# Performance work log

Hardware: AMD Instinct MI355X
Metric: run time of the kernel (lower is better)

The kernel has to match this reference:

```python
import jax, jax.numpy as jnp
import numpy as np

NC, CIN, COUT = 10000, 64, 64      # coarse points, inChans, outChans
CH = COUT // 2                     # up_conv / skip channels
NCONVS, TMP = 2, 2                 # nConvs, temp_mp_skip
GX = GY = GT = 64                  # coarse grid
FX, FY, FT = 2 * GX, 2 * GY, GT    # fine grid after [2,2,1] upsample
NF = 4 * NC                        # fine points (2x2x1 expansion per coarse voxel)
BN_EPS = 1e-5


def _build_maps():
    """Build MinkowskiEngine-style kernel maps (in_idx, out_idx) for a 3x3x3
    stride-1 sparse conv on the fine coordinate set. Padded with NF (dummy)."""
    rng = np.random.default_rng(0)
    lin = rng.choice(GX * GY * GT, size=NC, replace=False)
    cx, cy, ct = np.unravel_index(lin, (GX, GY, GT))
    coarse = np.stack([cx, cy, ct], 1).astype(np.int64)
    # transpose-conv output coords: each coarse voxel emits a 2x2x1 block,
    # offset order fixed and matched by the einsum in reference()
    offs4 = np.array([[0, 0, 0], [0, 1, 0], [1, 0, 0], [1, 1, 0]])
    fine = (coarse[:, None, :] * np.array([2, 2, 1]) + offs4[None]).reshape(-1, 3)
    table = -np.ones(FX * FY * FT, np.int64)
    keys = fine[:, 0] * (FY * FT) + fine[:, 1] * FT + fine[:, 2]
    table[keys] = np.arange(NF)
    offs = np.array([[dx, dy, dt] for dx in (-1, 0, 1)
                     for dy in (-1, 0, 1) for dt in (-1, 0, 1)])
    pin, pout = [], []
    for o in offs:
        nb = fine + o
        ok = (nb >= 0).all(1) & (nb[:, 0] < FX) & (nb[:, 1] < FY) & (nb[:, 2] < FT)
        k2 = np.clip(nb[:, 0] * (FY * FT) + nb[:, 1] * FT + nb[:, 2], 0, table.size - 1)
        idx = np.where(ok, table[k2], -1)
        m = idx >= 0
        pin.append(idx[m].astype(np.int32))
        pout.append(np.nonzero(m)[0].astype(np.int32))
    mmax = max(len(p) for p in pin)
    in_idx = np.full((27, mmax), NF, np.int32)
    out_idx = np.full((27, mmax), NF, np.int32)
    for k in range(27):
        n = len(pin[k])
        in_idx[k, :n] = pin[k]
        out_idx[k, :n] = pout[k]
    return jnp.asarray(in_idx), jnp.asarray(out_idx)


def sparse_conv(x, w, in_idx, out_idx):
    """gather -> GEMM -> scatter-add. x:[NF,Cin], w:[27,Cin,Cout]."""
    xp = jnp.concatenate([x, jnp.zeros((1, x.shape[1]), x.dtype)], 0)
    g = xp[in_idx]                                   # [27, M, Cin]
    c = jnp.einsum('kmc,kco->kmo', g, w)             # [27, M, Cout]
    out = jnp.zeros((NF + 1, w.shape[-1]), x.dtype)
    out = out.at[out_idx.reshape(-1)].add(c.reshape(-1, w.shape[-1]))
    return out[:NF]


def batch_norm(x, gamma, beta):
    m = x.mean(0)
    v = jnp.var(x, axis=0)
    return (x - m) * jax.lax.rsqrt(v + BN_EPS) * gamma + beta


def setup_inputs() -> dict:
    key = jax.random.key(0)
    ks = jax.random.split(key, 5)
    in_idx, out_idx = _build_maps()
    s = 0.05
    return {
        'x_feats': jax.random.normal(ks[0], (NC, CIN), jnp.float32),
        'skip_feats': jax.random.normal(ks[1], (NF * TMP, CH), jnp.float32),
        'w_up': jax.random.normal(ks[2], (4, CIN, CIN), jnp.float32) * s,
        'w_upconv': jax.random.normal(ks[3], (27, CIN, CH), jnp.float32) * s,
        'bn1_gamma': jnp.ones((CH,), jnp.float32),
        'bn1_beta': jnp.zeros((CH,), jnp.float32),
        'convs_w': jax.random.normal(ks[4], (NCONVS, 27, COUT, COUT), jnp.float32) * s,
        'convs_gamma': jnp.ones((NCONVS, COUT), jnp.float32),
        'convs_beta': jnp.zeros((NCONVS, COUT), jnp.float32),
        'in_idx': in_idx,
        'out_idx': out_idx,
    }


def reference(x_feats, skip_feats, w_up, w_upconv, bn1_gamma, bn1_beta,
              convs_w, convs_gamma, convs_beta, in_idx, out_idx):
    # MinkowskiConvolutionTranspose kernel=stride=[2,2,1]: each coarse point
    # emits 4 fine points (offset order matches _build_maps).
    up = jnp.einsum('nc,kco->nko', x_feats, w_up).reshape(NF, CIN)  # [NF, CIN]
    out = jax.nn.elu(batch_norm(sparse_conv(up, w_upconv, in_idx, out_idx),
                                bn1_gamma, bn1_beta))               # [NF, CH]
    # MinkowskiMaxPooling kernel=stride=[1,1,TMP] over the temporal axis
    skip = skip_feats.reshape(NF, TMP, CH).max(axis=1)              # [NF, CH]
    xcat = jnp.concatenate([out, skip], axis=1)                     # [NF, COUT]
    h = xcat
    for i in range(NCONVS):  # LUConv: ELU(BN(conv(x)))
        h = jax.nn.elu(batch_norm(sparse_conv(h, convs_w[i], in_idx, out_idx),
                                  convs_gamma[i], convs_beta[i]))
    return jax.nn.elu(h + xcat)
```

## Files before the change

### kernel.cpp

```cpp
#include <hip/hip_runtime.h>
#include <math.h>


__device__ __forceinline__ float elu(float v) { return v > 0.f ? v : expm1f(v); }

__device__ __forceinline__ float4 f4add(float4 a, float4 b) {
  return make_float4(a.x + b.x, a.y + b.y, a.z + b.z, a.w + b.w);
}

__global__ void __launch_bounds__(256) k_init(int* __restrict__ pos, float* __restrict__ stats,
                                              float* __restrict__ upz, float* __restrict__ xcz,
                                              int n_pos) {
  int i = blockIdx.x * blockDim.x + threadIdx.x;
  for (int j = i; j < n_pos; j += gridDim.x * blockDim.x) pos[j] = -1;
  if (i < 384) stats[i] = 0.f;
  if (i < 64) { upz[i] = 0.f; xcz[i] = 0.f; }
}

__global__ void k_meta(const int* __restrict__ in_idx, int mmax, int NF,
                       int* __restrict__ cnt, int* __restrict__ base) {
  __shared__ int sc[27];
  int k = threadIdx.x;
  if (k < 27) {
    int lo = 0, hi = mmax;
    while (lo < hi) {
      int mid = (lo + hi) >> 1;
      if (in_idx[(size_t)k * mmax + mid] >= NF) hi = mid; else lo = mid + 1;
    }
    sc[k] = lo;
    cnt[k] = lo;
  }
  __syncthreads();
  if (threadIdx.x == 0) {
    int acc = 0;
    for (int j = 0; j < 27; ++j) { base[j] = acc; acc += (sc[j] + 127) & ~127; }
    base[27] = acc;
  }
}

__global__ void __launch_bounds__(256) k_scatter(const int* __restrict__ out_idx, int mmax, int NF,
                                                 const int* __restrict__ cnt, const int* __restrict__ base,
                                                 int* __restrict__ pos) {
  int k = blockIdx.y;
  int m = blockIdx.x * blockDim.x + threadIdx.x;
  if (m >= cnt[k]) return;
  pos[(size_t)k * NF + out_idx[(size_t)k * mmax + m]] = base[k] + m;
}

template <int RU>
__global__ void __launch_bounds__(256) k_up(const float* __restrict__ x, const float* __restrict__ w_up,
                                            float* __restrict__ up, int NC) {
  const int lane = threadIdx.x & 63;
  const int j = threadIdx.x >> 6;
  float wreg[64];
#pragma unroll
  for (int ci = 0; ci < 64; ++ci) wreg[ci] = w_up[(size_t)(j * 64 + ci) * 64 + lane];
  const int n0 = blockIdx.x * RU;
#pragma unroll
  for (int r = 0; r < RU; ++r) {
    int n = n0 + r;
    if (n >= NC) break;
    const float* xr = x + (size_t)n * 64;
    float a0 = 0.f, a1 = 0.f, a2 = 0.f, a3 = 0.f;
#pragma unroll
    for (int ci = 0; ci < 64; ci += 4) {
      a0 = fmaf(xr[ci + 0], wreg[ci + 0], a0);
      a1 = fmaf(xr[ci + 1], wreg[ci + 1], a1);
      a2 = fmaf(xr[ci + 2], wreg[ci + 2], a2);
      a3 = fmaf(xr[ci + 3], wreg[ci + 3], a3);
    }
    up[(size_t)(n * 4 + j) * 64 + lane] = (a0 + a1) + (a2 + a3);
  }
}

template <int COUT>
__global__ void __launch_bounds__(256) k_gemm2(const float* __restrict__ x,
                                               const float* __restrict__ w,
                                               const int* __restrict__ in_idx, int mmax, int NF,
                                               const int* __restrict__ cnt, const int* __restrict__ base,
                                               float* __restrict__ Cbuf) {
  constexpr int CW = COUT / 16;
  constexpr int STA = 68;
  __shared__ float At[64 * STA];
  __shared__ float Ws[64 * COUT];
  __shared__ int sidx[64];

  const int k = blockIdx.y;
  const int ck = cnt[k];
  const int m0 = blockIdx.x * 64;
  if (m0 >= ck) return;
  const int tid = threadIdx.x;

  if (tid < 64) {
    int m = m0 + tid;
    sidx[tid] = (m < ck) ? in_idx[(size_t)k * mmax + m] : NF;
  }
  {
    const float4* wsrc = (const float4*)(w + (size_t)k * 64 * COUT);
    float4* wdst = (float4*)Ws;
#pragma unroll
    for (int p = 0; p < 64 * COUT / 4 / 256; ++p) wdst[tid + p * 256] = wsrc[tid + p * 256];
  }
  __syncthreads();
  {
    const int r0 = tid & 15;
    const int cb = tid >> 4;
#pragma unroll
    for (int p = 0; p < 4; ++p) {
      int row = r0 + p * 16;
      float4 v = *(const float4*)(x + (size_t)sidx[row] * 64 + cb * 4);
      At[(cb * 4 + 0) * STA + row] = v.x;
      At[(cb * 4 + 1) * STA + row] = v.y;
      At[(cb * 4 + 2) * STA + row] = v.z;
      At[(cb * 4 + 3) * STA + row] = v.w;
    }
  }
  __syncthreads();

  const int mi = tid >> 4;
  const int ci = tid & 15;
  float acc[4][CW];
#pragma unroll
  for (int i = 0; i < 4; ++i)
#pragma unroll
    for (int j = 0; j < CW; ++j) acc[i][j] = 0.f;

#pragma unroll 4
  for (int kk = 0; kk < 64; ++kk) {
    float4 a = *(const float4*)(At + kk * STA + mi * 4);
    const float* brow = Ws + kk * COUT + ci * CW;
    float b[CW];
#pragma unroll
    for (int j = 0; j < CW; ++j) b[j] = brow[j];
    float av[4] = {a.x, a.y, a.z, a.w};
#pragma unroll
    for (int i = 0; i < 4; ++i)
#pragma unroll
      for (int j = 0; j < CW; ++j) acc[i][j] = fmaf(av[i], b[j], acc[i][j]);
  }

  const int bk = base[k];
#pragma unroll
  for (int i = 0; i < 4; ++i) {
    float* dst = Cbuf + (size_t)(bk + m0 + mi * 4 + i) * COUT + ci * CW;
#pragma unroll
    for (int j = 0; j < CW; ++j) dst[j] = acc[i][j];
  }
}

template <int COUT>
__global__ void __launch_bounds__(256) k_red(const float* __restrict__ Cbuf, const int* __restrict__ pos,
                                             float* __restrict__ y, float* __restrict__ s1,
                                             float* __restrict__ s2, int NF) {
  constexpr int C4 = COUT / 4;
  const int c4 = threadIdx.x & (C4 - 1);
  const int rl = threadIdx.x / C4;
  const int rpb = 256 / C4;
  float4 p1 = make_float4(0, 0, 0, 0), p2 = make_float4(0, 0, 0, 0);
  for (int o = blockIdx.x * rpb + rl; o < NF; o += gridDim.x * rpb) {
    float4 acc = make_float4(0, 0, 0, 0);
#pragma unroll
    for (int k = 0; k < 27; ++k) {
      int p = pos[(size_t)k * NF + o];
      if (p >= 0) {
        float4 v = *(const float4*)(Cbuf + (size_t)p * COUT + c4 * 4);
        acc = f4add(acc, v);
      }
    }
    *(float4*)(y + (size_t)o * COUT + c4 * 4) = acc;
    p1 = f4add(p1, acc);
    p2 = f4add(p2, make_float4(acc.x * acc.x, acc.y * acc.y, acc.z * acc.z, acc.w * acc.w));
  }
  __shared__ float4 sh[256];
  sh[threadIdx.x] = p1;
  __syncthreads();
  if (rl == 0) {
    float4 t = make_float4(0, 0, 0, 0);
    for (int r = 0; r < rpb; ++r) t = f4add(t, sh[r * C4 + c4]);
    atomicAdd(s1 + c4 * 4 + 0, t.x); atomicAdd(s1 + c4 * 4 + 1, t.y);
    atomicAdd(s1 + c4 * 4 + 2, t.z); atomicAdd(s1 + c4 * 4 + 3, t.w);
  }
  __syncthreads();
  sh[threadIdx.x] = p2;
  __syncthreads();
  if (rl == 0) {
    float4 t = make_float4(0, 0, 0, 0);
    for (int r = 0; r < rpb; ++r) t = f4add(t, sh[r * C4 + c4]);
    atomicAdd(s2 + c4 * 4 + 0, t.x); atomicAdd(s2 + c4 * 4 + 1, t.y);
    atomicAdd(s2 + c4 * 4 + 2, t.z); atomicAdd(s2 + c4 * 4 + 3, t.w);
  }
}

__global__ void __launch_bounds__(256) k_xcat(const float* __restrict__ y1, const float* __restrict__ skip,
                                              const float* __restrict__ gamma, const float* __restrict__ beta,
                                              const float* __restrict__ s1, const float* __restrict__ s2,
                                              float* __restrict__ xcat, int NF) {
  int t = blockIdx.x * blockDim.x + threadIdx.x;
  if (t >= NF * 32) return;
  int c = t & 31, o = t >> 5;
  float invn = 1.f / (float)NF;
  float m = s1[c] * invn;
  float var = s2[c] * invn - m * m;
  float sc = rsqrtf(var + 1e-5f) * gamma[c];
  float v = (y1[(size_t)o * 32 + c] - m) * sc + beta[c];
  xcat[(size_t)o * 64 + c] = elu(v);
  float a = skip[((size_t)o * 2) * 32 + c];
  float b = skip[((size_t)o * 2 + 1) * 32 + c];
  xcat[(size_t)o * 64 + 32 + c] = fmaxf(a, b);
}

__global__ void __launch_bounds__(256) k_norm(const float* __restrict__ y, const float* __restrict__ gamma,
                                              const float* __restrict__ beta, const float* __restrict__ s1,
                                              const float* __restrict__ s2, float* __restrict__ h, int NF) {
  int t = blockIdx.x * blockDim.x + threadIdx.x;
  if (t >= NF * 64) return;
  int c = t & 63;
  float invn = 1.f / (float)NF;
  float m = s1[c] * invn;
  float var = s2[c] * invn - m * m;
  float sc = rsqrtf(var + 1e-5f) * gamma[c];
  h[t] = elu((y[t] - m) * sc + beta[c]);
}

__global__ void __launch_bounds__(256) k_final(const float* __restrict__ y, const float* __restrict__ gamma,
                                               const float* __restrict__ beta, const float* __restrict__ s1,
                                               const float* __restrict__ s2, const float* __restrict__ xcat,
                                               float* __restrict__ out, int NF) {
  int t = blockIdx.x * blockDim.x + threadIdx.x;
  if (t >= NF * 64) return;
  int c = t & 63;
  float invn = 1.f / (float)NF;
  float m = s1[c] * invn;
  float var = s2[c] * invn - m * m;
  float sc = rsqrtf(var + 1e-5f) * gamma[c];
  float v = elu((y[t] - m) * sc + beta[c]);
  out[t] = elu(v + xcat[t]);
}

extern "C" void kernel_launch(void* const* d_in, const int* in_sizes, int n_in,
                              void* d_out, int out_size, void* d_ws, size_t ws_size,
                              hipStream_t stream) {
  const float* x_feats  = (const float*)d_in[0];
  const float* skip     = (const float*)d_in[1];
  const float* w_up     = (const float*)d_in[2];
  const float* w_upconv = (const float*)d_in[3];
  const float* bn1_g    = (const float*)d_in[4];
  const float* bn1_b    = (const float*)d_in[5];
  const float* convs_w  = (const float*)d_in[6];
  const float* convs_g  = (const float*)d_in[7];
  const float* convs_b  = (const float*)d_in[8];
  const int*   in_idx   = (const int*)d_in[9];
  const int*   out_idx  = (const int*)d_in[10];

  const int NC = in_sizes[0] / 64;
  const int NF = 4 * NC;
  const int mmax = in_sizes[9] / 27;

  char* ws = (char*)d_ws;
  size_t off = 0;
  auto alloc = [&](size_t bytes) -> void* {
    void* p = ws + off;
    off += (bytes + 255) & ~(size_t)255;
    return p;
  };
  int*   pos   = (int*)alloc((size_t)27 * NF * 4);
  int*   cnt   = (int*)alloc(32 * 4);
  int*   basep = (int*)alloc(32 * 4);
  float* stats = (float*)alloc(384 * 4);
  float* up    = (float*)alloc(((size_t)NF + 1) * 64 * 4);
  float* xcat  = (float*)alloc(((size_t)NF + 1) * 64 * 4);
  float* y     = (float*)alloc((size_t)NF * 64 * 4);
  float* Cb    = (float*)(ws + off);
  float* h     = up;

  k_init<<<1024, 256, 0, stream>>>(pos, stats, up + (size_t)NF * 64,
                                   xcat + (size_t)NF * 64, 27 * NF);
  k_meta<<<1, 64, 0, stream>>>(in_idx, mmax, NF, cnt, basep);
  dim3 gs((mmax + 255) / 256, 27);
  k_scatter<<<gs, 256, 0, stream>>>(out_idx, mmax, NF, cnt, basep, pos);
  k_up<16><<<(NC + 15) / 16, 256, 0, stream>>>(x_feats, w_up, up, NC);

  dim3 gg((mmax + 63) / 64, 27);
  k_gemm2<32><<<gg, 256, 0, stream>>>(up, w_upconv, in_idx, mmax, NF, cnt, basep, Cb);
  k_red<32><<<320, 256, 0, stream>>>(Cb, pos, y, stats + 0, stats + 64, NF);
  k_xcat<<<(NF * 32 + 255) / 256, 256, 0, stream>>>(y, skip, bn1_g, bn1_b,
                                                    stats + 0, stats + 64, xcat, NF);
  k_gemm2<64><<<gg, 256, 0, stream>>>(xcat, convs_w, in_idx, mmax, NF, cnt, basep, Cb);
  k_red<64><<<640, 256, 0, stream>>>(Cb, pos, y, stats + 128, stats + 192, NF);
  k_norm<<<(NF * 64 + 255) / 256, 256, 0, stream>>>(y, convs_g, convs_b,
                                                    stats + 128, stats + 192, h, NF);
  k_gemm2<64><<<gg, 256, 0, stream>>>(h, convs_w + 27 * 64 * 64, in_idx, mmax, NF, cnt, basep, Cb);
  k_red<64><<<640, 256, 0, stream>>>(Cb, pos, y, stats + 256, stats + 320, NF);
  k_final<<<(NF * 64 + 255) / 256, 256, 0, stream>>>(y, convs_g + 64, convs_b + 64,
                                                     stats + 256, stats + 320, xcat,
                                                     (float*)d_out, NF);
}
```

Measured before the change: 459.6 us.

## Replace dense per-offset position map with compact per-output neighbor lists

The dense 27xNF position table, which needed filling with -1 and scanning over all 27 offsets for every output row, is replaced by a per-output degree counter plus a list of up to 32 neighbor entries built with atomics. The reduction kernels now loop only over the real neighbors of each output, cutting index reads and branches. Grid sizes for the reduction and init kernels also change so there is one row group per block. Atomic insertion makes the summation order nondeterministic, which can perturb floating-point results slightly, and the list size assumes at most 32 neighbors per output.

New measurement: 791.8 us. 1.72x slower.

```diff
diff --git a/kernel.cpp b/kernel.cpp
--- a/kernel.cpp
+++ b/kernel.cpp
@@ -8,11 +8,11 @@
   return make_float4(a.x + b.x, a.y + b.y, a.z + b.z, a.w + b.w);
 }
 
-__global__ void __launch_bounds__(256) k_init(int* __restrict__ pos, float* __restrict__ stats,
+__global__ void __launch_bounds__(256) k_init(int* __restrict__ deg, float* __restrict__ stats,
                                               float* __restrict__ upz, float* __restrict__ xcz,
-                                              int n_pos) {
+                                              int NF) {
   int i = blockIdx.x * blockDim.x + threadIdx.x;
-  for (int j = i; j < n_pos; j += gridDim.x * blockDim.x) pos[j] = -1;
+  for (int j = i; j < NF; j += gridDim.x * blockDim.x) deg[j] = 0;
   if (i < 384) stats[i] = 0.f;
   if (i < 64) { upz[i] = 0.f; xcz[i] = 0.f; }
 }
@@ -38,13 +38,15 @@
   }
 }
 
-__global__ void __launch_bounds__(256) k_scatter(const int* __restrict__ out_idx, int mmax, int NF,
-                                                 const int* __restrict__ cnt, const int* __restrict__ base,
-                                                 int* __restrict__ pos) {
+__global__ void __launch_bounds__(256) k_scatter2(const int* __restrict__ out_idx, int mmax,
+                                                  const int* __restrict__ cnt, const int* __restrict__ base,
+                                                  int* __restrict__ deg, int* __restrict__ ent) {
   int k = blockIdx.y;
   int m = blockIdx.x * blockDim.x + threadIdx.x;
   if (m >= cnt[k]) return;
-  pos[(size_t)k * NF + out_idx[(size_t)k * mmax + m]] = base[k] + m;
+  int o = out_idx[(size_t)k * mmax + m];
+  int s = atomicAdd(deg + o, 1);
+  ent[(size_t)o * 32 + s] = base[k] + m;
 }
 
 template <int RU>
@@ -149,23 +151,22 @@
 }
 
 template <int COUT>
-__global__ void __launch_bounds__(256) k_red(const float* __restrict__ Cbuf, const int* __restrict__ pos,
-                                             float* __restrict__ y, float* __restrict__ s1,
-                                             float* __restrict__ s2, int NF) {
+__global__ void __launch_bounds__(256) k_red2(const float* __restrict__ Cbuf, const int* __restrict__ deg,
+                                              const int* __restrict__ ent, float* __restrict__ y,
+                                              float* __restrict__ s1, float* __restrict__ s2, int NF) {
   constexpr int C4 = COUT / 4;
   const int c4 = threadIdx.x & (C4 - 1);
   const int rl = threadIdx.x / C4;
-  const int rpb = 256 / C4;
+  constexpr int rpb = 256 / C4;
   float4 p1 = make_float4(0, 0, 0, 0), p2 = make_float4(0, 0, 0, 0);
   for (int o = blockIdx.x * rpb + rl; o < NF; o += gridDim.x * rpb) {
+    const int d = deg[o];
+    const int* el = ent + (size_t)o * 32;
     float4 acc = make_float4(0, 0, 0, 0);
-#pragma unroll
-    for (int k = 0; k < 27; ++k) {
-      int p = pos[(size_t)k * NF + o];
-      if (p >= 0) {
-        float4 v = *(const float4*)(Cbuf + (size_t)p * COUT + c4 * 4);
-        acc = f4add(acc, v);
-      }
+    for (int j = 0; j < d; ++j) {
+      int p = el[j];
+      float4 v = *(const float4*)(Cbuf + (size_t)p * COUT + c4 * 4);
+      acc = f4add(acc, v);
     }
     *(float4*)(y + (size_t)o * COUT + c4 * 4) = acc;
     p1 = f4add(p1, acc);
@@ -263,7 +264,8 @@
     off += (bytes + 255) & ~(size_t)255;
     return p;
   };
-  int*   pos   = (int*)alloc((size_t)27 * NF * 4);
+  int*   deg   = (int*)alloc((size_t)NF * 4);
+  int*   ent   = (int*)alloc((size_t)NF * 32 * 4);
   int*   cnt   = (int*)alloc(32 * 4);
   int*   basep = (int*)alloc(32 * 4);
   float* stats = (float*)alloc(384 * 4);
@@ -273,24 +275,24 @@
   float* Cb    = (float*)(ws + off);
   float* h     = up;
 
-  k_init<<<1024, 256, 0, stream>>>(pos, stats, up + (size_t)NF * 64,
-                                   xcat + (size_t)NF * 64, 27 * NF);
+  k_init<<<160, 256, 0, stream>>>(deg, stats, up + (size_t)NF * 64,
+                                  xcat + (size_t)NF * 64, NF);
   k_meta<<<1, 64, 0, stream>>>(in_idx, mmax, NF, cnt, basep);
   dim3 gs((mmax + 255) / 256, 27);
-  k_scatter<<<gs, 256, 0, stream>>>(out_idx, mmax, NF, cnt, basep, pos);
+  k_scatter2<<<gs, 256, 0, stream>>>(out_idx, mmax, cnt, basep, deg, ent);
   k_up<16><<<(NC + 15) / 16, 256, 0, stream>>>(x_feats, w_up, up, NC);
 
   dim3 gg((mmax + 63) / 64, 27);
   k_gemm2<32><<<gg, 256, 0, stream>>>(up, w_upconv, in_idx, mmax, NF, cnt, basep, Cb);
-  k_red<32><<<320, 256, 0, stream>>>(Cb, pos, y, stats + 0, stats + 64, NF);
+  k_red2<32><<<(NF + 31) / 32, 256, 0, stream>>>(Cb, deg, ent, y, stats + 0, stats + 64, NF);
   k_xcat<<<(NF * 32 + 255) / 256, 256, 0, stream>>>(y, skip, bn1_g, bn1_b,
                                                     stats + 0, stats + 64, xcat, NF);
   k_gemm2<64><<<gg, 256, 0, stream>>>(xcat, convs_w, in_idx, mmax, NF, cnt, basep, Cb);
-  k_red<64><<<640, 256, 0, stream>>>(Cb, pos, y, stats + 128, stats + 192, NF);
+  k_red2<64><<<(NF + 15) / 16, 256, 0, stream>>>(Cb, deg, ent, y, stats + 128, stats + 192, NF);
   k_norm<<<(NF * 64 + 255) / 256, 256, 0, stream>>>(y, convs_g, convs_b,
                                                     stats + 128, stats + 192, h, NF);
   k_gemm2<64><<<gg, 256, 0, stream>>>(h, convs_w + 27 * 64 * 64, in_idx, mmax, NF, cnt, basep, Cb);
-  k_red<64><<<640, 256, 0, stream>>>(Cb, pos, y, stats + 256, stats + 320, NF);
+  k_red2<64><<<(NF + 15) / 16, 256, 0, stream>>>(Cb, deg, ent, y, stats + 256, stats + 320, NF);
   k_final<<<(NF * 64 + 255) / 256, 256, 0, stream>>>(y, convs_g + 64, convs_b + 64,
                                                      stats + 256, stats + 320, xcat,
                                                      (float*)d_out, NF);
```
